# Optimization experiments

Hardware: AMD Instinct MI355X
Metric: run time of the kernel (lower is better)

## Reference

```python
import jax, jax.numpy as jnp
import numpy as np

B = 1024
FEAT_C = [64, 64, 128, 256, 512]    # channel dim of each intermediate feature map
SPATIAL = [1024, 1024, 256, 64, 16]  # flattened HxW of each map (32x32 input)
STRIDES = [1, 1, 2, 4, 8]
NUM_CLASS = 10


def _conv(x, w, b, s):
    y = jax.lax.conv_general_dilated(x, w, (s, s), 'SAME',
                                     dimension_numbers=('NCHW', 'OIHW', 'NCHW'))
    return y + b[None, :, None, None]


def setup_inputs() -> dict:
    key = jax.random.key(0)
    ks = iter(jax.random.split(key, 64))
    nrm = lambda shape, scale=1.0: jax.random.normal(next(ks), shape, jnp.float32) * scale
    inp = {'x': nrm((B, 3, 32, 32))}
    inp['noise_w'] = nrm((15, 3, 3, 3), 0.1)
    inp['noise_b'] = nrm((15,), 0.01)
    for i, (c, s) in enumerate(zip(FEAT_C, SPATIAL)):
        inp[f'feat_w{i}'] = nrm((c, 3, 3, 3), 0.2)
        inp[f'feat_b{i}'] = nrm((c,), 0.01)
        inp[f'mu_w{i}'] = nrm((NUM_CLASS, s), 1.0 / np.sqrt(s))
        inp[f'mu_b{i}'] = nrm((NUM_CLASS,), 0.01)
        inp[f'std_w{i}'] = nrm((NUM_CLASS, s), 1.0 / np.sqrt(s))
        inp[f'std_b{i}'] = nrm((NUM_CLASS,), 0.01)
    inp['clf_w'] = nrm((1, 5), 0.5)
    inp['clf_b'] = nrm((1,), 0.01)
    return inp


def _forward(x, noise_w, noise_b, feat_ws, feat_bs, mu_ws, mu_bs, std_ws, std_bs, clf_w, clf_b):
    Bsz = x.shape[0]
    # noised_img = x.repeat([1,5,1,1]) + noise_layer(x)   -> [B,15,32,32]
    noised = jnp.tile(x, (1, 5, 1, 1)) + _conv(x, noise_w, noise_b, 1)
    ekey = jax.random.key(42)
    scores, means, stds = [], [], []
    for i in range(5):
        xi = noised[:, 3 * i:3 * (i + 1)]
        # stand-in for pretrained_model.intermediate_forward -> [B, C_i, S_i]
        f = _conv(xi, feat_ws[i], feat_bs[i], STRIDES[i]).reshape(Bsz, FEAT_C[i], -1)
        # Linear over flattened-spatial dim then transpose(1,2): [B, 10, C_i]
        x_mean = jnp.einsum('bcs,ks->bkc', f, mu_ws[i]) + mu_bs[i][None, :, None]
        x_std = jnp.einsum('bcs,ks->bkc', f, std_ws[i]) + std_bs[i][None, :, None]
        # original builds dense diag(std)^2 [B,10,C,C]; diagonal exploited analytically
        var = x_std * x_std                       # diag entries of x_variance (== scale_tril)
        eps = jax.random.normal(jax.random.fold_in(ekey, i), x_mean.shape, x_mean.dtype)
        d = var * eps                             # sample - mean = scale_tril @ eps (diagonal)
        # -0.5 * d^T inv(diag(var)) d, inverse done analytically instead of torch.inverse
        mahal = -0.5 * jnp.sum(d * d / var, axis=-1)   # [B, 10]
        idx = jnp.argmax(mahal, axis=1)
        scores.append(jnp.max(mahal, axis=1))
        means.append(jnp.take_along_axis(x_mean, idx[:, None, None], axis=1)[:, 0, :])
        stds.append(jnp.take_along_axis(x_std, idx[:, None, None], axis=1)[:, 0, :])
    score_stack = jnp.stack(scores, axis=1)       # [B, 5]
    out = (score_stack @ clf_w.T + clf_b)[:, 0]   # classifier Linear(5,1), squeeze(-1)
    return out, means, stds


def reference(x, noise_w, noise_b,
              feat_w0, feat_b0, mu_w0, mu_b0, std_w0, std_b0,
              feat_w1, feat_b1, mu_w1, mu_b1, std_w1, std_b1,
              feat_w2, feat_b2, mu_w2, mu_b2, std_w2, std_b2,
              feat_w3, feat_b3, mu_w3, mu_b3, std_w3, std_b3,
              feat_w4, feat_b4, mu_w4, mu_b4, std_w4, std_b4,
              clf_w, clf_b):
    feat_ws = [feat_w0, feat_w1, feat_w2, feat_w3, feat_w4]
    feat_bs = [feat_b0, feat_b1, feat_b2, feat_b3, feat_b4]
    mu_ws = [mu_w0, mu_w1, mu_w2, mu_w3, mu_w4]
    mu_bs = [mu_b0, mu_b1, mu_b2, mu_b3, mu_b4]
    std_ws = [std_w0, std_w1, std_w2, std_w3, std_w4]
    std_bs = [std_b0, std_b1, std_b2, std_b3, std_b4]
    out, means, stds = _forward(x, noise_w, noise_b, feat_ws, feat_bs,
                                mu_ws, mu_bs, std_ws, std_bs, clf_w, clf_b)
    return (out, *means, *stds)
```

## Files before the change

kernel.cpp:

```cpp
#include <hip/hip_runtime.h>
#include <cstdint>

#define B_SZ 1024
#define NTHR 640

__host__ __device__ inline void tf2x32(uint32_t k0, uint32_t k1,
                                       uint32_t x0, uint32_t x1,
                                       uint32_t& o0, uint32_t& o1) {
  uint32_t ks2 = 0x1BD11BDAu ^ k0 ^ k1;
#define TF_RND(r) { x0 += x1; x1 = (x1 << (r)) | (x1 >> (32 - (r))); x1 ^= x0; }
  x0 += k0; x1 += k1;
  TF_RND(13) TF_RND(15) TF_RND(26) TF_RND(6)
  x0 += k1; x1 += ks2 + 1u;
  TF_RND(17) TF_RND(29) TF_RND(16) TF_RND(24)
  x0 += ks2; x1 += k0 + 2u;
  TF_RND(13) TF_RND(15) TF_RND(26) TF_RND(6)
  x0 += k0; x1 += k1 + 3u;
  TF_RND(17) TF_RND(29) TF_RND(16) TF_RND(24)
  x0 += k1; x1 += ks2 + 4u;
  TF_RND(13) TF_RND(15) TF_RND(26) TF_RND(6)
  x0 += ks2; x1 += k0 + 5u;
#undef TF_RND
  o0 = x0; o1 = x1;
}

__device__ inline float erfinv_f32(float x) {
  float w = -log1pf(-x * x);
  float p;
  if (w < 5.0f) {
    w -= 2.5f;
    p = 2.81022636e-08f;
    p = fmaf(p, w, 3.43273939e-07f);
    p = fmaf(p, w, -3.5233877e-06f);
    p = fmaf(p, w, -4.39150654e-06f);
    p = fmaf(p, w, 0.00021858087f);
    p = fmaf(p, w, -0.00125372503f);
    p = fmaf(p, w, -0.00417768164f);
    p = fmaf(p, w, 0.246640727f);
    p = fmaf(p, w, 1.50140941f);
  } else {
    w = sqrtf(w) - 3.0f;
    p = -0.000200214257f;
    p = fmaf(p, w, 0.000100950558f);
    p = fmaf(p, w, 0.00134934322f);
    p = fmaf(p, w, -0.00367342844f);
    p = fmaf(p, w, 0.00573950773f);
    p = fmaf(p, w, -0.0076224613f);
    p = fmaf(p, w, 0.00943887047f);
    p = fmaf(p, w, 1.00167406f);
    p = fmaf(p, w, 2.83297682f);
  }
  return p * x;
}

__device__ inline float jax_normal_pt(uint32_t k0, uint32_t k1, uint32_t e) {
  uint32_t o0, o1;
  tf2x32(k0, k1, 0u, e, o0, o1);
  uint32_t bits = o0 ^ o1;
  float f = __uint_as_float((bits >> 9) | 0x3f800000u) - 1.0f;
  const float LO = -0.99999994f;
  float u = fmaxf(LO, fmaf(f, 2.0f, LO));
  return 1.41421356f * erfinv_f32(u);
}

struct OodArgs {
  const float* x;
  const float* noise_w;
  const float* noise_b;
  const float* feat_w[5];
  const float* feat_b[5];
  const float* mu_w[5];
  const float* mu_b[5];
  const float* std_w[5];
  const float* std_b[5];
  float* mean_out[5];
  float* std_out[5];
  float* scores;
  float* gws;
  uint32_t fk0[5], fk1[5];
};

#define PITCH 35
#define CHSZ  (34 * PITCH)
#define XSZ   (3 * CHSZ)

#define A_XP   0
#define A_XI   3570
#define A_NW   7140
#define A_NB   7221
#define A_SMEM 7224

template<int S, int STRIDE>
__device__ __forceinline__ void stageA(const OodArgs& A_, float* smem, int i) {
  constexpr int Wd = 32 / STRIDE;
  const int b = blockIdx.x;
  const int t = threadIdx.x;

  float* s_xp = smem + A_XP;
  float* s_xi = smem + A_XI;
  float* s_nw = smem + A_NW;
  float* s_nb = smem + A_NB;

  {
    float4 z; z.x = z.y = z.z = z.w = 0.0f;
    float4* z4 = (float4*)smem;
    for (int p = t; p < (2 * XSZ) / 4; p += NTHR) z4[p] = z;
  }
  if (t < 81) s_nw[t] = A_.noise_w[81 * i + t];
  if (t < 3)  s_nb[t] = A_.noise_b[3 * i + t];
  __syncthreads();
  const float* xb = A_.x + (size_t)b * 3072;
  for (int p = t; p < 3072; p += NTHR) {
    int ci = p >> 10, rr = p & 1023, yy = rr >> 5, xx = rr & 31;
    s_xp[ci * CHSZ + (yy + 1) * PITCH + (xx + 1)] = xb[p];
  }
  __syncthreads();

  if (t < 384) {
    const int co = t >> 7;
    const int r  = t & 127;
    const int y  = r >> 2;
    const int xs = (r & 3) * 8;
    const float nb = s_nb[co];
    float acc[8];
    #pragma unroll
    for (int j = 0; j < 8; ++j) acc[j] = nb;
    #pragma unroll
    for (int c2 = 0; c2 < 3; ++c2) {
      #pragma unroll
      for (int dy = 0; dy < 3; ++dy) {
        const float w0 = s_nw[co * 27 + c2 * 9 + dy * 3 + 0];
        const float w1 = s_nw[co * 27 + c2 * 9 + dy * 3 + 1];
        const float w2 = s_nw[co * 27 + c2 * 9 + dy * 3 + 2];
        const int ra = c2 * CHSZ + (y + dy) * PITCH + xs;
        float R[10];
        #pragma unroll
        for (int u = 0; u < 10; ++u) R[u] = s_xp[ra + u];
        #pragma unroll
        for (int j = 0; j < 8; ++j) {
          acc[j] = fmaf(w0, R[j],     acc[j]);
          acc[j] = fmaf(w1, R[j + 1], acc[j]);
          acc[j] = fmaf(w2, R[j + 2], acc[j]);
        }
      }
    }
    const int ob = co * CHSZ + (y + 1) * PITCH + (xs + 1);
    #pragma unroll
    for (int j = 0; j < 8; ++j)
      s_xi[ob + j] = acc[j] + s_xp[ob + j];
  }
  __syncthreads();

  const int G  = t >> 5;
  const int ss = t & 31;
  const int wh = G & 1;
  const int kk = G >> 1;
  const float* wsrc = (wh ? A_.std_w[i] : A_.mu_w[i]) + kk * S;
  float* gdst = A_.gws + (size_t)(b * 5 + i) * 560;

#define REDUCE_WRITE(ci_) { \
    _Pragma("unroll") \
    for (int j = 0; j < 9; ++j) { \
      float v = acc[j]; \
      v += __shfl_xor(v,  1, 64); \
      v += __shfl_xor(v,  2, 64); \
      v += __shfl_xor(v,  4, 64); \
      v += __shfl_xor(v,  8, 64); \
      v += __shfl_xor(v, 16, 64); \
      acc[j] = v; \
    } \
    if ((ci_) == 0) { \
      rs += __shfl_xor(rs, 1, 64); rs += __shfl_xor(rs, 2, 64); \
      rs += __shfl_xor(rs, 4, 64); rs += __shfl_xor(rs, 8, 64); \
      rs += __shfl_xor(rs, 16, 64); \
    } \
    if (ss == 0) { \
      _Pragma("unroll") \
      for (int j = 0; j < 9; ++j) \
        gdst[(wh * 10 + kk) * 27 + (ci_) * 9 + j] = acc[j]; \
      if ((ci_) == 0) gdst[540 + wh * 10 + kk] = rs; \
    } }

  if constexpr (STRIDE == 1) {
    const float* wr = wsrc + ss * 32;
    const int rbase0 = ss * PITCH;
    #pragma unroll
    for (int ci = 0; ci < 3; ++ci) {
      const int rb = ci * CHSZ + rbase0;
      float acc[9];
      #pragma unroll
      for (int j = 0; j < 9; ++j) acc[j] = 0.0f;
      float rs = 0.0f;
      float Av[3], Bv[3], Cv[3];
      #pragma unroll
      for (int u = 0; u < 3; ++u) {
        Av[u] = s_xi[rb + u * PITCH + 0];
        Bv[u] = s_xi[rb + u * PITCH + 1];
      }

#define WCOMP(V, L) ((L) == 0 ? (V).x : (L) == 1 ? (V).y : (L) == 2 ? (V).z : (V).w)
#define STEP(X, P, Q, R, W0) { \
    _Pragma("unroll") \
    for (int u = 0; u < 3; ++u) R[u] = s_xi[rb + u * PITCH + (X) + 2]; \
    const float w0c = WCOMP(W0, (X) & 3); \
    _Pragma("unroll") \
    for (int dy = 0; dy < 3; ++dy) { \
      acc[dy*3+0] = fmaf(w0c, P[dy], acc[dy*3+0]); \
      acc[dy*3+1] = fmaf(w0c, Q[dy], acc[dy*3+1]); \
      acc[dy*3+2] = fmaf(w0c, R[dy], acc[dy*3+2]); \
    } \
    if (ci == 0) rs += w0c; \
  }
#define G4_0(c) { const float4 w0 = *(const float4*)(wr + (c)); \
    STEP((c)+0, Av, Bv, Cv, w0) STEP((c)+1, Bv, Cv, Av, w0) \
    STEP((c)+2, Cv, Av, Bv, w0) STEP((c)+3, Av, Bv, Cv, w0) }
#define G4_1(c) { const float4 w0 = *(const float4*)(wr + (c)); \
    STEP((c)+0, Bv, Cv, Av, w0) STEP((c)+1, Cv, Av, Bv, w0) \
    STEP((c)+2, Av, Bv, Cv, w0) STEP((c)+3, Bv, Cv, Av, w0) }
#define G4_2(c) { const float4 w0 = *(const float4*)(wr + (c)); \
    STEP((c)+0, Cv, Av, Bv, w0) STEP((c)+1, Av, Bv, Cv, w0) \
    STEP((c)+2, Bv, Cv, Av, w0) STEP((c)+3, Cv, Av, Bv, w0) }

      G4_0(0) G4_1(4) G4_2(8) G4_0(12) G4_1(16) G4_2(20) G4_0(24) G4_1(28)

#undef G4_0
#undef G4_1
#undef G4_2
#undef STEP
#undef WCOMP
      REDUCE_WRITE(ci)
    }
  } else {
    constexpr int PER = (S >= 32) ? (S / 32) : 1;
    #pragma unroll
    for (int ci = 0; ci < 3; ++ci) {
      float acc[9];
      #pragma unroll
      for (int j = 0; j < 9; ++j) acc[j] = 0.0f;
      float rs = 0.0f;
      if (S >= 32 || ss < S) {
        #pragma unroll
        for (int u = 0; u < PER; ++u) {
          const int s  = (S >= 32) ? (ss * PER + u) : ss;
          const int yo = s / Wd, xo = s % Wd;
          const float wx = wsrc[s];
          #pragma unroll
          for (int dy = 0; dy < 3; ++dy) {
            const int ba = ci * CHSZ + (yo * STRIDE + dy + 1) * PITCH + (xo * STRIDE + 1);
            #pragma unroll
            for (int dx = 0; dx < 3; ++dx)
              acc[dy * 3 + dx] = fmaf(wx, s_xi[ba + dx], acc[dy * 3 + dx]);
          }
          if (ci == 0) rs += wx;
        }
      }
      REDUCE_WRITE(ci)
    }
  }
#undef REDUCE_WRITE
}

__global__ __launch_bounds__(NTHR, 4)
void ood_a_s1(OodArgs A_) {
  __shared__ __align__(16) float smem[A_SMEM];
  stageA<1024, 1>(A_, smem, blockIdx.y);
}

__global__ __launch_bounds__(NTHR, 4)
void ood_a_sN(OodArgs A_) {
  __shared__ __align__(16) float smem[A_SMEM];
  switch (blockIdx.y) {
    case 0:  stageA<256, 2>(A_, smem, 2); break;
    case 1:  stageA< 64, 4>(A_, smem, 3); break;
    default: stageA< 16, 8>(A_, smem, 4); break;
  }
}

template<int I, int C>
__device__ __forceinline__ void stageB(const OodArgs& A_, float* smem) {
  const int b = blockIdx.x;
  const int t = threadIdx.x;

  float* s_g   = smem;
  float* s_rs  = smem + 540;
  float* s_std = smem + 560;
  float* s_pt  = smem + 560 + 10 * C;
  int*   s_idx = (int*)(smem + 570 + 10 * C);

  const float* feat_w = A_.feat_w[I];
  const float* feat_b = A_.feat_b[I];
  const uint32_t fk0 = A_.fk0[I], fk1 = A_.fk1[I];

  const float* gsrc = A_.gws + (size_t)(b * 5 + I) * 560;
  for (int p = t; p < 560; p += 320) smem[p] = gsrc[p];
  __syncthreads();

  for (int v = t; v < 10 * C; v += 320) {
    const int k2 = v / C; const int c = v - k2 * C;
    const float* fw = feat_w + c * 27;
    float a2 = 0.0f;
    #pragma unroll
    for (int j = 0; j < 27; ++j) a2 = fmaf(s_g[(10 + k2) * 27 + j], fw[j], a2);
    a2 = fmaf(feat_b[c], s_rs[10 + k2], a2) + A_.std_b[I][k2];
    s_std[v] = a2;
  }
  __syncthreads();

  {
    const int g  = t >> 6;
    const int ln = t & 63;
    float m0 = 0.0f, m1 = 0.0f;
    for (int c = ln; c < C; c += 64) {
      {
        const float sd  = s_std[g * C + c];
        const float eps = jax_normal_pt(fk0, fk1, (uint32_t)((b * 10 + g) * C + c));
        m0 = fmaf(sd * sd, eps * eps, m0);
      }
      {
        const float sd  = s_std[(g + 5) * C + c];
        const float eps = jax_normal_pt(fk0, fk1, (uint32_t)((b * 10 + g + 5) * C + c));
        m1 = fmaf(sd * sd, eps * eps, m1);
      }
    }
    #pragma unroll
    for (int off = 32; off > 0; off >>= 1) {
      m0 += __shfl_down(m0, off, 64);
      m1 += __shfl_down(m1, off, 64);
    }
    if (ln == 0) { s_pt[g] = m0; s_pt[g + 5] = m1; }
  }
  __syncthreads();
  if (t == 0) {
    float best = -INFINITY; int bi = 0;
    #pragma unroll
    for (int k2 = 0; k2 < 10; ++k2) {
      float m = -0.5f * s_pt[k2];
      if (m > best) { best = m; bi = k2; }
    }
    A_.scores[b * 5 + I] = best;
    *s_idx = bi;
  }
  __syncthreads();

  const int idx = *s_idx;
  for (int c = t; c < C; c += 320) {
    const float* fw = feat_w + c * 27;
    float a1 = 0.0f;
    #pragma unroll
    for (int j = 0; j < 27; ++j) a1 = fmaf(s_g[idx * 27 + j], fw[j], a1);
    a1 = fmaf(feat_b[c], s_rs[idx], a1) + A_.mu_b[I][idx];
    A_.mean_out[I][(size_t)b * C + c] = a1;
    A_.std_out[I][(size_t)b * C + c]  = s_std[idx * C + c];
  }
}

__global__ __launch_bounds__(320)
void ood_b(OodArgs A_) {
  __shared__ float smem[571 + 5120];
  switch (blockIdx.y) {
    case 0: stageB<4, 512>(A_, smem); break;
    case 1: stageB<3, 256>(A_, smem); break;
    case 2: stageB<2, 128>(A_, smem); break;
    case 3: stageB<1,  64>(A_, smem); break;
    default: stageB<0, 64>(A_, smem); break;
  }
}

__global__ void ood_clf(const float* __restrict__ scores,
                        const float* __restrict__ clf_w,
                        const float* __restrict__ clf_b,
                        float* __restrict__ out) {
  int b = blockIdx.x * blockDim.x + threadIdx.x;
  if (b < B_SZ) {
    float acc = clf_b[0];
    #pragma unroll
    for (int i = 0; i < 5; ++i) acc = fmaf(scores[b * 5 + i], clf_w[i], acc);
    out[b] = acc;
  }
}

extern "C" void kernel_launch(void* const* d_in, const int* in_sizes, int n_in,
                              void* d_out, int out_size, void* d_ws, size_t ws_size,
                              hipStream_t stream) {
  (void)in_sizes; (void)n_in; (void)out_size; (void)ws_size;
  const float* clf_w = (const float*)d_in[33];
  const float* clf_b = (const float*)d_in[34];
  float* out = (float*)d_out;
  float* ws  = (float*)d_ws;

  OodArgs A_;
  A_.x       = (const float*)d_in[0];
  A_.noise_w = (const float*)d_in[1];
  A_.noise_b = (const float*)d_in[2];
  const size_t NMEAN = 1048576;
  const size_t moff[5] = {1024, 66560, 132096, 263168, 525312};
  for (int i = 0; i < 5; ++i) {
    A_.feat_w[i]   = (const float*)d_in[3 + 6 * i];
    A_.feat_b[i]   = (const float*)d_in[4 + 6 * i];
    A_.mu_w[i]     = (const float*)d_in[5 + 6 * i];
    A_.mu_b[i]     = (const float*)d_in[6 + 6 * i];
    A_.std_w[i]    = (const float*)d_in[7 + 6 * i];
    A_.std_b[i]    = (const float*)d_in[8 + 6 * i];
    A_.mean_out[i] = out + moff[i];
    A_.std_out[i]  = out + moff[i] + NMEAN;
    tf2x32(0u, 42u, 0u, (uint32_t)i, A_.fk0[i], A_.fk1[i]);
  }
  A_.scores = ws;
  A_.gws    = ws + 5120;

  ood_a_s1<<<dim3(B_SZ, 2), NTHR, 0, stream>>>(A_);
  ood_a_sN<<<dim3(B_SZ, 3), NTHR, 0, stream>>>(A_);
  ood_b<<<dim3(B_SZ, 5), 320, 0, stream>>>(A_);
  ood_clf<<<(B_SZ + 255) / 256, 256, 0, stream>>>(A_.scores, clf_w, clf_b, out);
}
```

Measured before the change: 275.4 us.

## Fuse stage B into stage A for strided branches, keep intermediates in LDS

For the three strided branches (i=2,3,4), the per-sample projection, std/mean computation, sampling and argmax are fused into a single kernel. The 560-float reduced gram vector stays in shared memory instead of being written to and reread from the global workspace. The stage-B kernel now handles only branches 0 and 1, which cuts its grid size and its shared-memory footprint. The fused kernel uses more shared memory and ordering changes, and the heavy stride-1 kernel now launches after the fused one.

```diff
diff --git a/kernel.cpp b/kernel.cpp
--- a/kernel.cpp
+++ b/kernel.cpp
@@ -89,13 +89,16 @@
 #define A_NW   7140
 #define A_NB   7221
 #define A_SMEM 7224
-
-template<int S, int STRIDE>
-__device__ __forceinline__ void stageA(const OodArgs& A_, float* smem, int i) {
-  constexpr int Wd = 32 / STRIDE;
-  const int b = blockIdx.x;
+#define F_G    7224
+#define F_RS   7764
+#define F_PT   7784
+#define F_IDX  7794
+#define F_SMEM 7795
+#define F_STD  0
+
+__device__ __forceinline__ void phases12(const OodArgs& A_, float* smem,
+                                         int i, int b) {
   const int t = threadIdx.x;
-
   float* s_xp = smem + A_XP;
   float* s_xi = smem + A_XI;
   float* s_nw = smem + A_NW;
@@ -150,15 +153,9 @@
       s_xi[ob + j] = acc[j] + s_xp[ob + j];
   }
   __syncthreads();
-
-  const int G  = t >> 5;
-  const int ss = t & 31;
-  const int wh = G & 1;
-  const int kk = G >> 1;
-  const float* wsrc = (wh ? A_.std_w[i] : A_.mu_w[i]) + kk * S;
-  float* gdst = A_.gws + (size_t)(b * 5 + i) * 560;
-
-#define REDUCE_WRITE(ci_) { \
+}
+
+#define REDUCE_WRITE(ci_, GD) { \
     _Pragma("unroll") \
     for (int j = 0; j < 9; ++j) { \
       float v = acc[j]; \
@@ -177,26 +174,41 @@
     if (ss == 0) { \
       _Pragma("unroll") \
       for (int j = 0; j < 9; ++j) \
-        gdst[(wh * 10 + kk) * 27 + (ci_) * 9 + j] = acc[j]; \
-      if ((ci_) == 0) gdst[540 + wh * 10 + kk] = rs; \
+        GD[(wh * 10 + kk) * 27 + (ci_) * 9 + j] = acc[j]; \
+      if ((ci_) == 0) GD[540 + wh * 10 + kk] = rs; \
     } }
 
-  if constexpr (STRIDE == 1) {
-    const float* wr = wsrc + ss * 32;
-    const int rbase0 = ss * PITCH;
-    #pragma unroll
-    for (int ci = 0; ci < 3; ++ci) {
-      const int rb = ci * CHSZ + rbase0;
-      float acc[9];
-      #pragma unroll
-      for (int j = 0; j < 9; ++j) acc[j] = 0.0f;
-      float rs = 0.0f;
-      float Av[3], Bv[3], Cv[3];
-      #pragma unroll
-      for (int u = 0; u < 3; ++u) {
-        Av[u] = s_xi[rb + u * PITCH + 0];
-        Bv[u] = s_xi[rb + u * PITCH + 1];
-      }
+__global__ __launch_bounds__(NTHR, 4)
+void ood_a_s1(OodArgs A_) {
+  __shared__ __align__(16) float smem[A_SMEM];
+  const int i = blockIdx.y;
+  const int b = blockIdx.x;
+  float* s_xi = smem + A_XI;
+  phases12(A_, smem, i, b);
+
+  const int t = threadIdx.x;
+  const int G  = t >> 5;
+  const int ss = t & 31;
+  const int wh = G & 1;
+  const int kk = G >> 1;
+  const float* wsrc = (wh ? A_.std_w[i] : A_.mu_w[i]) + kk * 1024;
+  float* gdst = A_.gws + (size_t)(b * 2 + i) * 560;
+
+  const float* wr = wsrc + ss * 32;
+  const int rbase0 = ss * PITCH;
+  #pragma unroll
+  for (int ci = 0; ci < 3; ++ci) {
+    const int rb = ci * CHSZ + rbase0;
+    float acc[9];
+    #pragma unroll
+    for (int j = 0; j < 9; ++j) acc[j] = 0.0f;
+    float rs = 0.0f;
+    float Av[3], Bv[3], Cv[3];
+    #pragma unroll
+    for (int u = 0; u < 3; ++u) {
+      Av[u] = s_xi[rb + u * PITCH + 0];
+      Bv[u] = s_xi[rb + u * PITCH + 1];
+    }
 
 #define WCOMP(V, L) ((L) == 0 ? (V).x : (L) == 1 ? (V).y : (L) == 2 ? (V).z : (V).w)
 #define STEP(X, P, Q, R, W0) { \
@@ -221,77 +233,147 @@
     STEP((c)+0, Cv, Av, Bv, w0) STEP((c)+1, Av, Bv, Cv, w0) \
     STEP((c)+2, Bv, Cv, Av, w0) STEP((c)+3, Cv, Av, Bv, w0) }
 
-      G4_0(0) G4_1(4) G4_2(8) G4_0(12) G4_1(16) G4_2(20) G4_0(24) G4_1(28)
+    G4_0(0) G4_1(4) G4_2(8) G4_0(12) G4_1(16) G4_2(20) G4_0(24) G4_1(28)
 
 #undef G4_0
 #undef G4_1
 #undef G4_2
 #undef STEP
 #undef WCOMP
-      REDUCE_WRITE(ci)
-    }
-  } else {
-    constexpr int PER = (S >= 32) ? (S / 32) : 1;
-    #pragma unroll
-    for (int ci = 0; ci < 3; ++ci) {
-      float acc[9];
+    REDUCE_WRITE(ci, gdst)
+  }
+}
+
+template<int I, int S, int STRIDE, int C>
+__device__ __forceinline__ void fused_body(const OodArgs& A_, float* smem) {
+  constexpr int Wd = 32 / STRIDE;
+  const int b = blockIdx.x;
+  const int t = threadIdx.x;
+  float* s_xi = smem + A_XI;
+  float* s_g  = smem + F_G;
+  float* s_rs = smem + F_RS;
+
+  phases12(A_, smem, I, b);
+
+  const int G  = t >> 5;
+  const int ss = t & 31;
+  const int wh = G & 1;
+  const int kk = G >> 1;
+  const float* wsrc = (wh ? A_.std_w[I] : A_.mu_w[I]) + kk * S;
+  constexpr int PER = (S >= 32) ? (S / 32) : 1;
+  #pragma unroll
+  for (int ci = 0; ci < 3; ++ci) {
+    float acc[9];
+    #pragma unroll
+    for (int j = 0; j < 9; ++j) acc[j] = 0.0f;
+    float rs = 0.0f;
+    if (S >= 32 || ss < S) {
       #pragma unroll
-      for (int j = 0; j < 9; ++j) acc[j] = 0.0f;
-      float rs = 0.0f;
-      if (S >= 32 || ss < S) {
+      for (int u = 0; u < PER; ++u) {
+        const int s  = (S >= 32) ? (ss * PER + u) : ss;
+        const int yo = s / Wd, xo = s % Wd;
+        const float wx = wsrc[s];
         #pragma unroll
-        for (int u = 0; u < PER; ++u) {
-          const int s  = (S >= 32) ? (ss * PER + u) : ss;
-          const int yo = s / Wd, xo = s % Wd;
-          const float wx = wsrc[s];
+        for (int dy = 0; dy < 3; ++dy) {
+          const int ba = ci * CHSZ + (yo * STRIDE + dy + 1) * PITCH + (xo * STRIDE + 1);
           #pragma unroll
-          for (int dy = 0; dy < 3; ++dy) {
-            const int ba = ci * CHSZ + (yo * STRIDE + dy + 1) * PITCH + (xo * STRIDE + 1);
-            #pragma unroll
-            for (int dx = 0; dx < 3; ++dx)
-              acc[dy * 3 + dx] = fmaf(wx, s_xi[ba + dx], acc[dy * 3 + dx]);
-          }
-          if (ci == 0) rs += wx;
+          for (int dx = 0; dx < 3; ++dx)
+            acc[dy * 3 + dx] = fmaf(wx, s_xi[ba + dx], acc[dy * 3 + dx]);
         }
+        if (ci == 0) rs += wx;
       }
-      REDUCE_WRITE(ci)
-    }
-  }
-#undef REDUCE_WRITE
+    }
+    REDUCE_WRITE(ci, s_g)
+  }
+  __syncthreads();
+
+  float* s_std = smem + F_STD;
+  float* s_pt  = smem + F_PT;
+  int*   s_idx = (int*)(smem + F_IDX);
+  const float* feat_w = A_.feat_w[I];
+  const float* feat_b = A_.feat_b[I];
+  const uint32_t fk0 = A_.fk0[I], fk1 = A_.fk1[I];
+
+  for (int v = t; v < 10 * C; v += NTHR) {
+    const int k2 = v / C; const int c = v & (C - 1);
+    const float* fw = feat_w + c * 27;
+    float a2 = 0.0f;
+    #pragma unroll
+    for (int j = 0; j < 27; ++j) a2 = fmaf(s_g[(10 + k2) * 27 + j], fw[j], a2);
+    a2 = fmaf(feat_b[c], s_rs[10 + k2], a2) + A_.std_b[I][k2];
+    s_std[v] = a2;
+  }
+  __syncthreads();
+
+  {
+    const int g  = t >> 6;
+    const int ln = t & 63;
+    float m0 = 0.0f;
+    for (int c = ln; c < C; c += 64) {
+      const float sd  = s_std[g * C + c];
+      const float eps = jax_normal_pt(fk0, fk1, (uint32_t)((b * 10 + g) * C + c));
+      m0 = fmaf(sd * sd, eps * eps, m0);
+    }
+    #pragma unroll
+    for (int off = 32; off > 0; off >>= 1) m0 += __shfl_down(m0, off, 64);
+    if (ln == 0) s_pt[g] = m0;
+  }
+  __syncthreads();
+  if (t == 0) {
+    float best = -INFINITY; int bi = 0;
+    #pragma unroll
+    for (int k2 = 0; k2 < 10; ++k2) {
+      float m = -0.5f * s_pt[k2];
+      if (m > best) { best = m; bi = k2; }
+    }
+    A_.scores[b * 5 + I] = best;
+    *s_idx = bi;
+  }
+  __syncthreads();
+
+  const int idx = *s_idx;
+  float* mo = A_.mean_out[I];
+  float* so = A_.std_out[I];
+  const float mb   = A_.mu_b[I][idx];
+  const float rs0v = s_rs[idx];
+  for (int c = t; c < C; c += NTHR) {
+    const float* fw = feat_w + c * 27;
+    float a1 = 0.0f;
+    #pragma unroll
+    for (int j = 0; j < 27; ++j) a1 = fmaf(s_g[idx * 27 + j], fw[j], a1);
+    a1 = fmaf(feat_b[c], rs0v, a1) + mb;
+    mo[(size_t)b * C + c] = a1;
+    so[(size_t)b * C + c] = s_std[idx * C + c];
+  }
 }
 
 __global__ __launch_bounds__(NTHR, 4)
-void ood_a_s1(OodArgs A_) {
-  __shared__ __align__(16) float smem[A_SMEM];
-  stageA<1024, 1>(A_, smem, blockIdx.y);
-}
-
-__global__ __launch_bounds__(NTHR, 4)
-void ood_a_sN(OodArgs A_) {
-  __shared__ __align__(16) float smem[A_SMEM];
+void ood_fused_sN(OodArgs A_) {
+  __shared__ __align__(16) float smem[F_SMEM];
   switch (blockIdx.y) {
-    case 0:  stageA<256, 2>(A_, smem, 2); break;
-    case 1:  stageA< 64, 4>(A_, smem, 3); break;
-    default: stageA< 16, 8>(A_, smem, 4); break;
-  }
-}
-
-template<int I, int C>
-__device__ __forceinline__ void stageB(const OodArgs& A_, float* smem) {
+    case 0:  fused_body<4,  16, 8, 512>(A_, smem); break;
+    case 1:  fused_body<3,  64, 4, 256>(A_, smem); break;
+    default: fused_body<2, 256, 2, 128>(A_, smem); break;
+  }
+}
+
+template<int I>
+__device__ __forceinline__ void stageB01(const OodArgs& A_, float* smem) {
+  constexpr int C = 64;
   const int b = blockIdx.x;
   const int t = threadIdx.x;
 
   float* s_g   = smem;
   float* s_rs  = smem + 540;
   float* s_std = smem + 560;
-  float* s_pt  = smem + 560 + 10 * C;
-  int*   s_idx = (int*)(smem + 570 + 10 * C);
+  float* s_pt  = smem + 1200;
+  int*   s_idx = (int*)(smem + 1210);
 
   const float* feat_w = A_.feat_w[I];
   const float* feat_b = A_.feat_b[I];
   const uint32_t fk0 = A_.fk0[I], fk1 = A_.fk1[I];
 
-  const float* gsrc = A_.gws + (size_t)(b * 5 + I) * 560;
+  const float* gsrc = A_.gws + (size_t)(b * 2 + I) * 560;
   for (int p = t; p < 560; p += 320) smem[p] = gsrc[p];
   __syncthreads();
 
@@ -355,15 +437,10 @@
 }
 
 __global__ __launch_bounds__(320)
-void ood_b(OodArgs A_) {
-  __shared__ float smem[571 + 5120];
-  switch (blockIdx.y) {
-    case 0: stageB<4, 512>(A_, smem); break;
-    case 1: stageB<3, 256>(A_, smem); break;
-    case 2: stageB<2, 128>(A_, smem); break;
-    case 3: stageB<1,  64>(A_, smem); break;
-    default: stageB<0, 64>(A_, smem); break;
-  }
+void ood_b01(OodArgs A_) {
+  __shared__ float smem[1211];
+  if (blockIdx.y == 0) stageB01<0>(A_, smem);
+  else                 stageB01<1>(A_, smem);
 }
 
 __global__ void ood_clf(const float* __restrict__ scores,
@@ -408,8 +485,8 @@
   A_.scores = ws;
   A_.gws    = ws + 5120;
 
+  ood_fused_sN<<<dim3(B_SZ, 3), NTHR, 0, stream>>>(A_);
   ood_a_s1<<<dim3(B_SZ, 2), NTHR, 0, stream>>>(A_);
-  ood_a_sN<<<dim3(B_SZ, 3), NTHR, 0, stream>>>(A_);
-  ood_b<<<dim3(B_SZ, 5), 320, 0, stream>>>(A_);
+  ood_b01<<<dim3(B_SZ, 2), 320, 0, stream>>>(A_);
   ood_clf<<<(B_SZ + 255) / 256, 256, 0, stream>>>(A_.scores, clf_w, clf_b, out);
 }
```

New measurement: 304.9 us. +10.7%, slower.
